# Kernel optimization log

Measured on AMD Instinct MI355X. Metric: run time of the kernel, lower is better.

Reference implementation:

```python
import jax, jax.numpy as jnp
from jax import lax
import numpy as np

GAMMA, ALPHA, BETA, THETA = 0.5, 0.5, 1.0, 1.0
BLOCK = 512  # tile size over the p2 point dim for the streaming K=1 knn


def _min_sqdist(p1, p2):
    """K=1 knn_points: min squared distance from each p1 point to p2. (B,N1,3),(B,N2,3) -> (B,N1).
    Streams p2 in blocks with a running min, never materializing the full NxM matrix."""
    B, N2, _ = p2.shape
    nb = N2 // BLOCK
    p2b = jnp.transpose(p2.reshape(B, nb, BLOCK, 3), (1, 0, 2, 3))  # (nb,B,BLOCK,3)
    p1sq = jnp.sum(p1 * p1, axis=-1)  # (B,N1)

    def step(carry, chunk):
        # ||a-b||^2 = ||a||^2 - 2 a.b + ||b||^2
        d = (p1sq[:, :, None]
             - 2.0 * jnp.einsum('bnd,bmd->bnm', p1, chunk)
             + jnp.sum(chunk * chunk, axis=-1)[:, None, :])
        return jnp.minimum(carry, jnp.min(d, axis=-1)), None

    init = jnp.full(p1sq.shape, jnp.inf, dtype=p1.dtype)
    out, _ = lax.scan(step, init, p2b)
    return out


def _pnt2quat(grasp_pred):
    center = grasp_pred[..., :3]
    q = grasp_pred[..., 3:]
    q = q / jnp.sqrt(jnp.sum(q * q, axis=-1, keepdims=True) + 1e-12)
    return center, q


def _mat2quat(g):
    R = g[..., :3, :3]
    t = g[..., :3, 3]
    tr = R[..., 0, 0] + R[..., 1, 1] + R[..., 2, 2]
    w = 0.5 * jnp.sqrt(jnp.maximum(1.0 + tr, 1e-12))
    inv4w = 1.0 / (4.0 * w)
    x = (R[..., 2, 1] - R[..., 1, 2]) * inv4w
    y = (R[..., 0, 2] - R[..., 2, 0]) * inv4w
    z = (R[..., 1, 0] - R[..., 0, 1]) * inv4w
    q = jnp.stack([w, x, y, z], axis=-1)
    return t, q


def setup_inputs() -> dict:
    key = jax.random.key(0)
    ks = jax.random.split(key, 8)
    B, N, M = 4, 16384, 2048
    xyz = jax.random.normal(ks[0], (B, N, 3), dtype=jnp.float32)
    sample_xyz = jax.random.normal(ks[1], (B, M, 3), dtype=jnp.float32)
    temp = jnp.asarray(0.5, dtype=jnp.float32)
    grasp_pred = jax.random.normal(ks[2], (B, M, 7), dtype=jnp.float32)
    # build valid SE(3) ground-truth grasps: rotation from unit quaternion (w>=0) + translation
    q = jax.random.normal(ks[3], (B, M, 4), dtype=jnp.float32)
    q = q / jnp.sqrt(jnp.sum(q * q, axis=-1, keepdims=True) + 1e-12)
    q = jnp.where(q[..., :1] < 0, -q, q)
    w, x, y, z = q[..., 0], q[..., 1], q[..., 2], q[..., 3]
    R = jnp.stack([
        jnp.stack([1 - 2 * (y * y + z * z), 2 * (x * y - w * z), 2 * (x * z + w * y)], -1),
        jnp.stack([2 * (x * y + w * z), 1 - 2 * (x * x + z * z), 2 * (y * z - w * x)], -1),
        jnp.stack([2 * (x * z - w * y), 2 * (y * z + w * x), 1 - 2 * (x * x + y * y)], -1),
    ], -2)  # (B,M,3,3)
    t = jax.random.normal(ks[4], (B, M, 3), dtype=jnp.float32)
    top = jnp.concatenate([R, t[..., None]], axis=-1)  # (B,M,3,4)
    bottom = jnp.broadcast_to(jnp.array([0., 0., 0., 1.], jnp.float32), (B, M, 1, 4))
    grasp_gt = jnp.concatenate([top, bottom], axis=-2)  # (B,M,4,4)
    class_pred = jax.random.uniform(ks[5], (B, M), dtype=jnp.float32, minval=1e-4, maxval=1.0 - 1e-4)
    class_gt = (jax.random.uniform(ks[6], (B, M)) < 0.5).astype(jnp.float32)
    return {"xyz": xyz, "sample_xyz": sample_xyz, "temp": temp, "grasp_pred": grasp_pred,
            "grasp_gt": grasp_gt, "class_pred": class_pred, "class_gt": class_gt}


def reference(xyz, sample_xyz, temp, grasp_pred, grasp_gt, class_pred, class_gt):
    # sample loss (chamfer-style with K=1 knn in both directions + max-min coverage term)
    d_smp_org = _min_sqdist(sample_xyz, xyz)   # (B,M)
    d_org_smp = _min_sqdist(xyz, sample_xyz)   # (B,N)
    sample_loss = (jnp.mean(d_smp_org)
                   + jnp.mean(jnp.max(d_smp_org, axis=-1))
                   + GAMMA * jnp.mean(d_org_smp))
    # projection loss
    proj_loss = temp ** 2
    center_pred, quat_pred = _pnt2quat(grasp_pred)
    center_gt, quat_gt = _mat2quat(grasp_gt)
    cls_w = class_gt.reshape(-1)
    dist = jnp.linalg.norm(center_pred.reshape(-1, 3) - center_gt.reshape(-1, 3) + 1e-6, axis=-1)
    trans_loss = jnp.mean(dist * cls_w)
    dot = jnp.sum(quat_pred.reshape(-1, 4) * quat_gt.reshape(-1, 4), axis=-1)
    rot = jnp.arccos(jnp.clip(jnp.abs(dot), 0.0, 1.0 - 1e-7))
    rot_loss = jnp.mean(rot * cls_w)
    reg_loss = trans_loss + ALPHA * rot_loss
    # classification loss (BCE on probabilities)
    p = jnp.clip(class_pred, 1e-7, 1.0 - 1e-7)
    cls_loss = -jnp.mean(class_gt * jnp.log(p) + (1.0 - class_gt) * jnp.log(1.0 - p))
    return THETA * sample_loss + proj_loss + BETA * reg_loss + cls_loss
```

## Files before the change

### kernel.cpp

```cpp
#include <hip/hip_runtime.h>
#include <math.h>

#define BB 4
#define NN 16384
#define MM 2048
#define BM (BB*MM)
#define BN (BB*NN)

#define TGT 256
#define S1  64
#define S2  8

#define PART1OFF 0
#define PART2OFF (S1*BM)
#define REDOFF   (PART1OFF + S1*BM + S2*BN)
#define R_SUMS1  (REDOFF)
#define R_MAXES  (REDOFF+32)
#define R_SUMS2  (REDOFF+64)
#define R_GST    (REDOFF+128)
#define R_GSR    (REDOFF+160)
#define R_GSC    (REDOFF+192)

__global__ __launch_bounds__(256) void k_min(const float* __restrict__ xyz,
                                             const float* __restrict__ smp,
                                             float* __restrict__ ws) {
    __shared__ float4 tgt[TGT];
    const int tid = threadIdx.x;
    const int bx  = blockIdx.x;
    const float* qptr; const float* tptr; float* outp;
    if (bx < 256) {
        int b = bx >> 6, r = bx & 63, qb = r >> 3, s = r & 7;
        int gq = b * NN + qb * 2048;
        qptr = xyz + (size_t)gq * 3;
        tptr = smp + (size_t)(b * MM + s * TGT) * 3;
        outp = ws + PART2OFF + s * BN + gq;
    } else {
        int bx2 = bx - 256;
        int b = bx2 >> 6, s = bx2 & 63;
        int gq = b * MM;
        qptr = smp + (size_t)gq * 3;
        tptr = xyz + (size_t)(b * NN + s * TGT) * 3;
        outp = ws + PART1OFF + s * BM + gq;
    }
    {
        float x = tptr[3*tid], y = tptr[3*tid+1], z = tptr[3*tid+2];
        tgt[tid] = make_float4(-2.0f*x, -2.0f*y, -2.0f*z, x*x + y*y + z*z);
    }
    float qx[8], qy[8], qz[8], mn[8];
#pragma unroll
    for (int k = 0; k < 8; ++k) {
        int q = tid + k * 256;
        qx[k] = qptr[3*q]; qy[k] = qptr[3*q+1]; qz[k] = qptr[3*q+2];
        mn[k] = INFINITY;
    }
    __syncthreads();
#pragma unroll 2
    for (int j = 0; j < TGT; j += 2) {
        float4 ta = tgt[j], tb = tgt[j+1];
#pragma unroll
        for (int k = 0; k < 8; ++k) {
            float da = fmaf(ta.x, qx[k], fmaf(ta.y, qy[k], fmaf(ta.z, qz[k], ta.w)));
            float db = fmaf(tb.x, qx[k], fmaf(tb.y, qy[k], fmaf(tb.z, qz[k], tb.w)));
            mn[k] = fminf(mn[k], fminf(da, db));
        }
    }
#pragma unroll
    for (int k = 0; k < 8; ++k) {
        int q = tid + k * 256;
        outp[q] = mn[k] + (qx[k]*qx[k] + qy[k]*qy[k] + qz[k]*qz[k]);
    }
}

__device__ __forceinline__ float blockSum256(float v, volatile float* s4) {
#pragma unroll
    for (int o = 32; o > 0; o >>= 1) v += __shfl_down(v, o, 64);
    __syncthreads();
    int lane = threadIdx.x & 63, w = threadIdx.x >> 6;
    if (lane == 0) s4[w] = v;
    __syncthreads();
    return s4[0] + s4[1] + s4[2] + s4[3];
}

__device__ __forceinline__ float blockMax256(float v, volatile float* s4) {
#pragma unroll
    for (int o = 32; o > 0; o >>= 1) v = fmaxf(v, __shfl_down(v, o, 64));
    __syncthreads();
    int lane = threadIdx.x & 63, w = threadIdx.x >> 6;
    if (lane == 0) s4[w] = v;
    __syncthreads();
    return fmaxf(fmaxf(s4[0], s4[1]), fmaxf(s4[2], s4[3]));
}

__global__ __launch_bounds__(256) void k_reduce(const float* __restrict__ gp,
                                                const float* __restrict__ gg,
                                                const float* __restrict__ cp,
                                                const float* __restrict__ cg,
                                                float* __restrict__ ws) {
    __shared__ float s4a[4], s4b[4], s4c[4];
    const int bx = blockIdx.x, tid = threadIdx.x;
    if (bx < 32) {
        int q = bx * 256 + tid;
        float v = INFINITY;
#pragma unroll
        for (int sp = 0; sp < S1; ++sp) v = fminf(v, ws[PART1OFF + sp * BM + q]);
        float bs = blockSum256(v, s4a);
        float bm = blockMax256(v, s4b);
        if (tid == 0) { ws[R_SUMS1 + bx] = bs; ws[R_MAXES + bx] = bm; }
    } else if (bx < 96) {
        int i = bx - 32;
        float s = 0.0f;
#pragma unroll
        for (int k = 0; k < 4; ++k) {
            int q = i * 1024 + tid + k * 256;
            float v = INFINITY;
#pragma unroll
            for (int sp = 0; sp < S2; ++sp) v = fminf(v, ws[PART2OFF + sp * BN + q]);
            s += v;
        }
        float bs = blockSum256(s, s4a);
        if (tid == 0) ws[R_SUMS2 + i] = bs;
    } else {
        int m = (bx - 96) * 256 + tid;
        const float* g = gp + (size_t)m * 7;
        float cxp = g[0], cyp = g[1], czp = g[2];
        float q0 = g[3], q1 = g[4], q2 = g[5], q3 = g[6];
        float invq = 1.0f / sqrtf(q0*q0 + q1*q1 + q2*q2 + q3*q3 + 1e-12f);
        const float* G = gg + (size_t)m * 16;
        float tr = G[0] + G[5] + G[10];
        float w = 0.5f * sqrtf(fmaxf(1.0f + tr, 1e-12f));
        float inv4w = 1.0f / (4.0f * w);
        float gqx = (G[9] - G[6]) * inv4w;
        float gqy = (G[2] - G[8]) * inv4w;
        float gqz = (G[4] - G[1]) * inv4w;
        float cw = cg[m];
        float dx = cxp - G[3]  + 1e-6f;
        float dy = cyp - G[7]  + 1e-6f;
        float dz = czp - G[11] + 1e-6f;
        float dist = sqrtf(dx*dx + dy*dy + dz*dz);
        float dot = (q0*w + q1*gqx + q2*gqy + q3*gqz) * invq;
        float rot = acosf(fminf(fabsf(dot), 1.0f - 1e-7f));
        float p = fminf(fmaxf(cp[m], 1e-7f), 1.0f - 1e-7f);
        float ce = cw * logf(p) + (1.0f - cw) * logf(1.0f - p);
        float s1 = blockSum256(dist * cw, s4a);
        float s2 = blockSum256(rot  * cw, s4b);
        float s3 = blockSum256(ce, s4c);
        int i = bx - 96;
        if (tid == 0) { ws[R_GST + i] = s1; ws[R_GSR + i] = s2; ws[R_GSC + i] = s3; }
    }
}

__global__ __launch_bounds__(256) void k_final(const float* __restrict__ temp,
                                               const float* __restrict__ ws,
                                               float* __restrict__ out) {
    __shared__ float s4[4];
    const int tid = threadIdx.x;
    float a = (tid < 32) ? ws[R_SUMS1 + tid] : 0.0f;
    float f = 0.0f;
    if (tid < 4) {
        f = -INFINITY;
#pragma unroll
        for (int r = 0; r < 8; ++r) f = fmaxf(f, ws[R_MAXES + tid * 8 + r]);
    }
    float b = (tid < 64) ? ws[R_SUMS2 + tid] : 0.0f;
    float c = (tid < 32) ? ws[R_GST + tid] : 0.0f;
    float d = (tid < 32) ? ws[R_GSR + tid] : 0.0f;
    float e = (tid < 32) ? ws[R_GSC + tid] : 0.0f;
    float A = blockSum256(a, s4);
    float F = blockSum256(f, s4);
    float B = blockSum256(b, s4);
    float C = blockSum256(c, s4);
    float D = blockSum256(d, s4);
    float E = blockSum256(e, s4);
    if (tid == 0) {
        float sample = A * (1.0f / BM) + F * 0.25f + 0.5f * B * (1.0f / BN);
        float reg    = C * (1.0f / BM) + 0.5f * D * (1.0f / BM);
        float cls    = -E * (1.0f / BM);
        float t = temp[0];
        out[0] = sample + t * t + reg + cls;
    }
}

extern "C" void kernel_launch(void* const* d_in, const int* in_sizes, int n_in,
                              void* d_out, int out_size, void* d_ws, size_t ws_size,
                              hipStream_t stream) {
    const float* xyz  = (const float*)d_in[0];
    const float* smp  = (const float*)d_in[1];
    const float* temp = (const float*)d_in[2];
    const float* gp   = (const float*)d_in[3];
    const float* gg   = (const float*)d_in[4];
    const float* cp   = (const float*)d_in[5];
    const float* cg   = (const float*)d_in[6];
    float* ws  = (float*)d_ws;
    float* out = (float*)d_out;

    hipLaunchKernelGGL(k_min,    dim3(512), dim3(256), 0, stream, xyz, smp, ws);
    hipLaunchKernelGGL(k_reduce, dim3(128), dim3(256), 0, stream, gp, gg, cp, cg, ws);
    hipLaunchKernelGGL(k_final,  dim3(1),   dim3(256), 0, stream, temp, ws, out);
}
```

Measured before the change: 97.38 us.

## Use packed FP32 FMAs in knn kernel and fuse final reduction via last-block atomic

The distance inner loop now processes query points in pairs with inline-asm v_pk_fma_f32, using op_sel to broadcast target components, so the FMA instruction count is halved. The separate single-block final kernel is removed. Instead, the last k_reduce block to finish, found with an atomic counter and threadfences, does the final sum. This saves one kernel launch and its tail. The counter is reset inside k_min, and the packed asm relies on correct op_sel semantics.

```diff
diff --git a/kernel.cpp b/kernel.cpp
--- a/kernel.cpp
+++ b/kernel.cpp
@@ -20,6 +20,28 @@
 #define R_GST    (REDOFF+128)
 #define R_GSR    (REDOFF+160)
 #define R_GSC    (REDOFF+192)
+#define R_CNT    (REDOFF+224)
+
+typedef float f2 __attribute__((ext_vector_type(2)));
+
+__device__ __forceinline__ f2 pk_fma_zw(f2 tzw, f2 q) {
+    f2 d;
+    asm("v_pk_fma_f32 %0, %1, %2, %1 op_sel:[0,0,1] op_sel_hi:[0,1,1]"
+        : "=v"(d) : "v"(tzw), "v"(q));
+    return d;
+}
+__device__ __forceinline__ f2 pk_fma_hi(f2 txy, f2 q, f2 c) {
+    f2 d;
+    asm("v_pk_fma_f32 %0, %1, %2, %3 op_sel:[1,0,0] op_sel_hi:[1,1,1]"
+        : "=v"(d) : "v"(txy), "v"(q), "v"(c));
+    return d;
+}
+__device__ __forceinline__ f2 pk_fma_lo(f2 txy, f2 q, f2 c) {
+    f2 d;
+    asm("v_pk_fma_f32 %0, %1, %2, %3 op_sel:[0,0,0] op_sel_hi:[0,1,1]"
+        : "=v"(d) : "v"(txy), "v"(q), "v"(c));
+    return d;
+}
 
 __global__ __launch_bounds__(256) void k_min(const float* __restrict__ xyz,
                                              const float* __restrict__ smp,
@@ -27,6 +49,7 @@
     __shared__ float4 tgt[TGT];
     const int tid = threadIdx.x;
     const int bx  = blockIdx.x;
+    if (bx == 0 && tid == 0) ((unsigned*)ws)[R_CNT] = 0u;
     const float* qptr; const float* tptr; float* outp;
     if (bx < 256) {
         int b = bx >> 6, r = bx & 63, qb = r >> 3, s = r & 7;
@@ -46,28 +69,40 @@
         float x = tptr[3*tid], y = tptr[3*tid+1], z = tptr[3*tid+2];
         tgt[tid] = make_float4(-2.0f*x, -2.0f*y, -2.0f*z, x*x + y*y + z*z);
     }
-    float qx[8], qy[8], qz[8], mn[8];
-#pragma unroll
-    for (int k = 0; k < 8; ++k) {
-        int q = tid + k * 256;
-        qx[k] = qptr[3*q]; qy[k] = qptr[3*q+1]; qz[k] = qptr[3*q+2];
-        mn[k] = INFINITY;
-    }
-    __syncthreads();
+    f2 qx2[4], qy2[4], qz2[4], mn2[4];
+#pragma unroll
+    for (int p = 0; p < 4; ++p) {
+        int qa = tid + (2*p)   * 256;
+        int qb = tid + (2*p+1) * 256;
+        qx2[p] = (f2){qptr[3*qa],   qptr[3*qb]};
+        qy2[p] = (f2){qptr[3*qa+1], qptr[3*qb+1]};
+        qz2[p] = (f2){qptr[3*qa+2], qptr[3*qb+2]};
+        mn2[p] = (f2){INFINITY, INFINITY};
+    }
+    __syncthreads();
+    const f2* tg2 = (const f2*)tgt;
 #pragma unroll 2
     for (int j = 0; j < TGT; j += 2) {
-        float4 ta = tgt[j], tb = tgt[j+1];
-#pragma unroll
-        for (int k = 0; k < 8; ++k) {
-            float da = fmaf(ta.x, qx[k], fmaf(ta.y, qy[k], fmaf(ta.z, qz[k], ta.w)));
-            float db = fmaf(tb.x, qx[k], fmaf(tb.y, qy[k], fmaf(tb.z, qz[k], tb.w)));
-            mn[k] = fminf(mn[k], fminf(da, db));
-        }
-    }
-#pragma unroll
-    for (int k = 0; k < 8; ++k) {
-        int q = tid + k * 256;
-        outp[q] = mn[k] + (qx[k]*qx[k] + qy[k]*qy[k] + qz[k]*qz[k]);
+        f2 taxy = tg2[2*j+0], tazw = tg2[2*j+1];
+        f2 tbxy = tg2[2*j+2], tbzw = tg2[2*j+3];
+#pragma unroll
+        for (int p = 0; p < 4; ++p) {
+            f2 da = pk_fma_zw(tazw, qz2[p]);
+            da = pk_fma_hi(taxy, qy2[p], da);
+            da = pk_fma_lo(taxy, qx2[p], da);
+            f2 db = pk_fma_zw(tbzw, qz2[p]);
+            db = pk_fma_hi(tbxy, qy2[p], db);
+            db = pk_fma_lo(tbxy, qx2[p], db);
+            mn2[p].x = fminf(mn2[p].x, fminf(da.x, db.x));
+            mn2[p].y = fminf(mn2[p].y, fminf(da.y, db.y));
+        }
+    }
+#pragma unroll
+    for (int p = 0; p < 4; ++p) {
+        int qa = tid + (2*p)   * 256;
+        int qb = tid + (2*p+1) * 256;
+        outp[qa] = mn2[p].x + (qx2[p].x*qx2[p].x + qy2[p].x*qy2[p].x + qz2[p].x*qz2[p].x);
+        outp[qb] = mn2[p].y + (qx2[p].y*qx2[p].y + qy2[p].y*qy2[p].y + qz2[p].y*qz2[p].y);
     }
 }
 
@@ -95,8 +130,11 @@
                                                 const float* __restrict__ gg,
                                                 const float* __restrict__ cp,
                                                 const float* __restrict__ cg,
-                                                float* __restrict__ ws) {
+                                                const float* __restrict__ temp,
+                                                float* __restrict__ ws,
+                                                float* __restrict__ out) {
     __shared__ float s4a[4], s4b[4], s4c[4];
+    __shared__ bool amLast;
     const int bx = blockIdx.x, tid = threadIdx.x;
     if (bx < 32) {
         int q = bx * 256 + tid;
@@ -147,36 +185,38 @@
         int i = bx - 96;
         if (tid == 0) { ws[R_GST + i] = s1; ws[R_GSR + i] = s2; ws[R_GSC + i] = s3; }
     }
-}
-
-__global__ __launch_bounds__(256) void k_final(const float* __restrict__ temp,
-                                               const float* __restrict__ ws,
-                                               float* __restrict__ out) {
-    __shared__ float s4[4];
-    const int tid = threadIdx.x;
-    float a = (tid < 32) ? ws[R_SUMS1 + tid] : 0.0f;
-    float f = 0.0f;
-    if (tid < 4) {
-        f = -INFINITY;
-#pragma unroll
-        for (int r = 0; r < 8; ++r) f = fmaxf(f, ws[R_MAXES + tid * 8 + r]);
-    }
-    float b = (tid < 64) ? ws[R_SUMS2 + tid] : 0.0f;
-    float c = (tid < 32) ? ws[R_GST + tid] : 0.0f;
-    float d = (tid < 32) ? ws[R_GSR + tid] : 0.0f;
-    float e = (tid < 32) ? ws[R_GSC + tid] : 0.0f;
-    float A = blockSum256(a, s4);
-    float F = blockSum256(f, s4);
-    float B = blockSum256(b, s4);
-    float C = blockSum256(c, s4);
-    float D = blockSum256(d, s4);
-    float E = blockSum256(e, s4);
+    __threadfence();
     if (tid == 0) {
-        float sample = A * (1.0f / BM) + F * 0.25f + 0.5f * B * (1.0f / BN);
-        float reg    = C * (1.0f / BM) + 0.5f * D * (1.0f / BM);
-        float cls    = -E * (1.0f / BM);
-        float t = temp[0];
-        out[0] = sample + t * t + reg + cls;
+        unsigned prev = atomicAdd((unsigned*)ws + R_CNT, 1u);
+        amLast = (prev == 127u);
+    }
+    __syncthreads();
+    if (amLast) {
+        __threadfence();
+        float a = (tid < 32) ? ws[R_SUMS1 + tid] : 0.0f;
+        float f = 0.0f;
+        if (tid < 4) {
+            f = -INFINITY;
+#pragma unroll
+            for (int r = 0; r < 8; ++r) f = fmaxf(f, ws[R_MAXES + tid * 8 + r]);
+        }
+        float b = (tid < 64) ? ws[R_SUMS2 + tid] : 0.0f;
+        float c = (tid < 32) ? ws[R_GST + tid] : 0.0f;
+        float d = (tid < 32) ? ws[R_GSR + tid] : 0.0f;
+        float e = (tid < 32) ? ws[R_GSC + tid] : 0.0f;
+        float A = blockSum256(a, s4a);
+        float F = blockSum256(f, s4a);
+        float B = blockSum256(b, s4a);
+        float C = blockSum256(c, s4a);
+        float D = blockSum256(d, s4a);
+        float E = blockSum256(e, s4a);
+        if (tid == 0) {
+            float sample = A * (1.0f / BM) + F * 0.25f + 0.5f * B * (1.0f / BN);
+            float reg    = C * (1.0f / BM) + 0.5f * D * (1.0f / BM);
+            float cls    = -E * (1.0f / BM);
+            float t = temp[0];
+            out[0] = sample + t * t + reg + cls;
+        }
     }
 }
 
@@ -194,6 +234,5 @@
     float* out = (float*)d_out;
 
     hipLaunchKernelGGL(k_min,    dim3(512), dim3(256), 0, stream, xyz, smp, ws);
-    hipLaunchKernelGGL(k_reduce, dim3(128), dim3(256), 0, stream, gp, gg, cp, cg, ws);
-    hipLaunchKernelGGL(k_final,  dim3(1),   dim3(256), 0, stream, temp, ws, out);
-}
+    hipLaunchKernelGGL(k_reduce, dim3(128), dim3(256), 0, stream, gp, gg, cp, cg, temp, ws, out);
+}
```

Measured after the change: 109.4 us. +12.3%, slower.

## Fuse grasp loss into min kernel and finalize via last-block atomic counter

Applied to the files above, without the earlier changes.

Moves the per-grasp regression and classification loss blocks into the knn min kernel as 32 extra blocks, and merges the final scalar reduction into the reduce kernel using a threadfence plus atomic counter so the last block finishes. This cuts the launch count from three to two and spreads the partial-min reduction over more blocks (128 instead of 64 for the N side). The counter is reset by block 0 of the first kernel, which relies on stream ordering, and the added fences and atomics add some overhead.

```diff
diff --git a/kernel.cpp b/kernel.cpp
--- a/kernel.cpp
+++ b/kernel.cpp
@@ -17,110 +17,46 @@
 #define R_SUMS1  (REDOFF)
 #define R_MAXES  (REDOFF+32)
 #define R_SUMS2  (REDOFF+64)
-#define R_GST    (REDOFF+128)
-#define R_GSR    (REDOFF+160)
-#define R_GSC    (REDOFF+192)
+#define R_GST    (REDOFF+192)
+#define R_GSR    (REDOFF+224)
+#define R_GSC    (REDOFF+256)
+#define R_CNT    (REDOFF+288)
+
+__device__ __forceinline__ float blockSum256(float v, volatile float* s4) {
+#pragma unroll
+    for (int o = 32; o > 0; o >>= 1) v += __shfl_down(v, o, 64);
+    __syncthreads();
+    int lane = threadIdx.x & 63, w = threadIdx.x >> 6;
+    if (lane == 0) s4[w] = v;
+    __syncthreads();
+    return s4[0] + s4[1] + s4[2] + s4[3];
+}
+
+__device__ __forceinline__ float blockMax256(float v, volatile float* s4) {
+#pragma unroll
+    for (int o = 32; o > 0; o >>= 1) v = fmaxf(v, __shfl_down(v, o, 64));
+    __syncthreads();
+    int lane = threadIdx.x & 63, w = threadIdx.x >> 6;
+    if (lane == 0) s4[w] = v;
+    __syncthreads();
+    return fmaxf(fmaxf(s4[0], s4[1]), fmaxf(s4[2], s4[3]));
+}
 
 __global__ __launch_bounds__(256) void k_min(const float* __restrict__ xyz,
                                              const float* __restrict__ smp,
+                                             const float* __restrict__ gp,
+                                             const float* __restrict__ gg,
+                                             const float* __restrict__ cp,
+                                             const float* __restrict__ cg,
                                              float* __restrict__ ws) {
     __shared__ float4 tgt[TGT];
+    __shared__ float s4a[4], s4b[4], s4c[4];
     const int tid = threadIdx.x;
     const int bx  = blockIdx.x;
-    const float* qptr; const float* tptr; float* outp;
-    if (bx < 256) {
-        int b = bx >> 6, r = bx & 63, qb = r >> 3, s = r & 7;
-        int gq = b * NN + qb * 2048;
-        qptr = xyz + (size_t)gq * 3;
-        tptr = smp + (size_t)(b * MM + s * TGT) * 3;
-        outp = ws + PART2OFF + s * BN + gq;
-    } else {
-        int bx2 = bx - 256;
-        int b = bx2 >> 6, s = bx2 & 63;
-        int gq = b * MM;
-        qptr = smp + (size_t)gq * 3;
-        tptr = xyz + (size_t)(b * NN + s * TGT) * 3;
-        outp = ws + PART1OFF + s * BM + gq;
-    }
-    {
-        float x = tptr[3*tid], y = tptr[3*tid+1], z = tptr[3*tid+2];
-        tgt[tid] = make_float4(-2.0f*x, -2.0f*y, -2.0f*z, x*x + y*y + z*z);
-    }
-    float qx[8], qy[8], qz[8], mn[8];
-#pragma unroll
-    for (int k = 0; k < 8; ++k) {
-        int q = tid + k * 256;
-        qx[k] = qptr[3*q]; qy[k] = qptr[3*q+1]; qz[k] = qptr[3*q+2];
-        mn[k] = INFINITY;
-    }
-    __syncthreads();
-#pragma unroll 2
-    for (int j = 0; j < TGT; j += 2) {
-        float4 ta = tgt[j], tb = tgt[j+1];
-#pragma unroll
-        for (int k = 0; k < 8; ++k) {
-            float da = fmaf(ta.x, qx[k], fmaf(ta.y, qy[k], fmaf(ta.z, qz[k], ta.w)));
-            float db = fmaf(tb.x, qx[k], fmaf(tb.y, qy[k], fmaf(tb.z, qz[k], tb.w)));
-            mn[k] = fminf(mn[k], fminf(da, db));
-        }
-    }
-#pragma unroll
-    for (int k = 0; k < 8; ++k) {
-        int q = tid + k * 256;
-        outp[q] = mn[k] + (qx[k]*qx[k] + qy[k]*qy[k] + qz[k]*qz[k]);
-    }
-}
-
-__device__ __forceinline__ float blockSum256(float v, volatile float* s4) {
-#pragma unroll
-    for (int o = 32; o > 0; o >>= 1) v += __shfl_down(v, o, 64);
-    __syncthreads();
-    int lane = threadIdx.x & 63, w = threadIdx.x >> 6;
-    if (lane == 0) s4[w] = v;
-    __syncthreads();
-    return s4[0] + s4[1] + s4[2] + s4[3];
-}
-
-__device__ __forceinline__ float blockMax256(float v, volatile float* s4) {
-#pragma unroll
-    for (int o = 32; o > 0; o >>= 1) v = fmaxf(v, __shfl_down(v, o, 64));
-    __syncthreads();
-    int lane = threadIdx.x & 63, w = threadIdx.x >> 6;
-    if (lane == 0) s4[w] = v;
-    __syncthreads();
-    return fmaxf(fmaxf(s4[0], s4[1]), fmaxf(s4[2], s4[3]));
-}
-
-__global__ __launch_bounds__(256) void k_reduce(const float* __restrict__ gp,
-                                                const float* __restrict__ gg,
-                                                const float* __restrict__ cp,
-                                                const float* __restrict__ cg,
-                                                float* __restrict__ ws) {
-    __shared__ float s4a[4], s4b[4], s4c[4];
-    const int bx = blockIdx.x, tid = threadIdx.x;
-    if (bx < 32) {
-        int q = bx * 256 + tid;
-        float v = INFINITY;
-#pragma unroll
-        for (int sp = 0; sp < S1; ++sp) v = fminf(v, ws[PART1OFF + sp * BM + q]);
-        float bs = blockSum256(v, s4a);
-        float bm = blockMax256(v, s4b);
-        if (tid == 0) { ws[R_SUMS1 + bx] = bs; ws[R_MAXES + bx] = bm; }
-    } else if (bx < 96) {
-        int i = bx - 32;
-        float s = 0.0f;
-#pragma unroll
-        for (int k = 0; k < 4; ++k) {
-            int q = i * 1024 + tid + k * 256;
-            float v = INFINITY;
-#pragma unroll
-            for (int sp = 0; sp < S2; ++sp) v = fminf(v, ws[PART2OFF + sp * BN + q]);
-            s += v;
-        }
-        float bs = blockSum256(s, s4a);
-        if (tid == 0) ws[R_SUMS2 + i] = bs;
-    } else {
-        int m = (bx - 96) * 256 + tid;
+    if (bx == 0 && tid == 0) ((unsigned*)ws)[R_CNT] = 0u;
+
+    if (bx >= 512) {
+        int m = (bx - 512) * 256 + tid;
         const float* g = gp + (size_t)m * 7;
         float cxp = g[0], cyp = g[1], czp = g[2];
         float q0 = g[3], q1 = g[4], q2 = g[5], q3 = g[6];
@@ -144,39 +80,115 @@
         float s1 = blockSum256(dist * cw, s4a);
         float s2 = blockSum256(rot  * cw, s4b);
         float s3 = blockSum256(ce, s4c);
-        int i = bx - 96;
+        int i = bx - 512;
         if (tid == 0) { ws[R_GST + i] = s1; ws[R_GSR + i] = s2; ws[R_GSC + i] = s3; }
-    }
-}
-
-__global__ __launch_bounds__(256) void k_final(const float* __restrict__ temp,
-                                               const float* __restrict__ ws,
-                                               float* __restrict__ out) {
-    __shared__ float s4[4];
-    const int tid = threadIdx.x;
-    float a = (tid < 32) ? ws[R_SUMS1 + tid] : 0.0f;
-    float f = 0.0f;
-    if (tid < 4) {
-        f = -INFINITY;
-#pragma unroll
-        for (int r = 0; r < 8; ++r) f = fmaxf(f, ws[R_MAXES + tid * 8 + r]);
-    }
-    float b = (tid < 64) ? ws[R_SUMS2 + tid] : 0.0f;
-    float c = (tid < 32) ? ws[R_GST + tid] : 0.0f;
-    float d = (tid < 32) ? ws[R_GSR + tid] : 0.0f;
-    float e = (tid < 32) ? ws[R_GSC + tid] : 0.0f;
-    float A = blockSum256(a, s4);
-    float F = blockSum256(f, s4);
-    float B = blockSum256(b, s4);
-    float C = blockSum256(c, s4);
-    float D = blockSum256(d, s4);
-    float E = blockSum256(e, s4);
+        return;
+    }
+
+    const float* qptr; const float* tptr; float* outp;
+    if (bx < 256) {
+        int b = bx >> 6, r = bx & 63, qb = r >> 3, s = r & 7;
+        int gq = b * NN + qb * 2048;
+        qptr = xyz + (size_t)gq * 3;
+        tptr = smp + (size_t)(b * MM + s * TGT) * 3;
+        outp = ws + PART2OFF + s * BN + gq;
+    } else {
+        int bx2 = bx - 256;
+        int b = bx2 >> 6, s = bx2 & 63;
+        int gq = b * MM;
+        qptr = smp + (size_t)gq * 3;
+        tptr = xyz + (size_t)(b * NN + s * TGT) * 3;
+        outp = ws + PART1OFF + s * BM + gq;
+    }
+    {
+        float x = tptr[3*tid], y = tptr[3*tid+1], z = tptr[3*tid+2];
+        tgt[tid] = make_float4(-2.0f*x, -2.0f*y, -2.0f*z, x*x + y*y + z*z);
+    }
+    float qx[8], qy[8], qz[8], mn[8];
+#pragma unroll
+    for (int k = 0; k < 8; ++k) {
+        int q = tid + k * 256;
+        qx[k] = qptr[3*q]; qy[k] = qptr[3*q+1]; qz[k] = qptr[3*q+2];
+        mn[k] = INFINITY;
+    }
+    __syncthreads();
+#pragma unroll 2
+    for (int j = 0; j < TGT; j += 2) {
+        float4 ta = tgt[j], tb = tgt[j+1];
+#pragma unroll
+        for (int k = 0; k < 8; ++k) {
+            float da = fmaf(ta.x, qx[k], fmaf(ta.y, qy[k], fmaf(ta.z, qz[k], ta.w)));
+            float db = fmaf(tb.x, qx[k], fmaf(tb.y, qy[k], fmaf(tb.z, qz[k], tb.w)));
+            mn[k] = fminf(mn[k], fminf(da, db));
+        }
+    }
+#pragma unroll
+    for (int k = 0; k < 8; ++k) {
+        int q = tid + k * 256;
+        outp[q] = mn[k] + (qx[k]*qx[k] + qy[k]*qy[k] + qz[k]*qz[k]);
+    }
+}
+
+__global__ __launch_bounds__(256) void k_reduce(const float* __restrict__ temp,
+                                                float* __restrict__ ws,
+                                                float* __restrict__ out) {
+    __shared__ float s4a[4], s4b[4];
+    __shared__ bool amLast;
+    const int bx = blockIdx.x, tid = threadIdx.x;
+    if (bx < 32) {
+        int q = bx * 256 + tid;
+        float v = INFINITY;
+#pragma unroll
+        for (int sp = 0; sp < S1; ++sp) v = fminf(v, ws[PART1OFF + sp * BM + q]);
+        float bs = blockSum256(v, s4a);
+        float bm = blockMax256(v, s4b);
+        if (tid == 0) { ws[R_SUMS1 + bx] = bs; ws[R_MAXES + bx] = bm; }
+    } else {
+        int i = bx - 32;
+        float s = 0.0f;
+#pragma unroll
+        for (int k = 0; k < 2; ++k) {
+            int q = i * 512 + tid + k * 256;
+            float v = INFINITY;
+#pragma unroll
+            for (int sp = 0; sp < S2; ++sp) v = fminf(v, ws[PART2OFF + sp * BN + q]);
+            s += v;
+        }
+        float bs = blockSum256(s, s4a);
+        if (tid == 0) ws[R_SUMS2 + i] = bs;
+    }
+    __threadfence();
     if (tid == 0) {
-        float sample = A * (1.0f / BM) + F * 0.25f + 0.5f * B * (1.0f / BN);
-        float reg    = C * (1.0f / BM) + 0.5f * D * (1.0f / BM);
-        float cls    = -E * (1.0f / BM);
-        float t = temp[0];
-        out[0] = sample + t * t + reg + cls;
+        unsigned prev = atomicAdd((unsigned*)ws + R_CNT, 1u);
+        amLast = (prev == 159u);
+    }
+    __syncthreads();
+    if (amLast) {
+        __threadfence();
+        float a = (tid < 32) ? ws[R_SUMS1 + tid] : 0.0f;
+        float f = 0.0f;
+        if (tid < 4) {
+            f = -INFINITY;
+#pragma unroll
+            for (int r = 0; r < 8; ++r) f = fmaxf(f, ws[R_MAXES + tid * 8 + r]);
+        }
+        float b = (tid < 128) ? ws[R_SUMS2 + tid] : 0.0f;
+        float c = (tid < 32) ? ws[R_GST + tid] : 0.0f;
+        float d = (tid < 32) ? ws[R_GSR + tid] : 0.0f;
+        float e = (tid < 32) ? ws[R_GSC + tid] : 0.0f;
+        float A = blockSum256(a, s4a);
+        float F = blockSum256(f, s4a);
+        float B = blockSum256(b, s4a);
+        float C = blockSum256(c, s4a);
+        float D = blockSum256(d, s4a);
+        float E = blockSum256(e, s4a);
+        if (tid == 0) {
+            float sample = A * (1.0f / BM) + F * 0.25f + 0.5f * B * (1.0f / BN);
+            float reg    = C * (1.0f / BM) + 0.5f * D * (1.0f / BM);
+            float cls    = -E * (1.0f / BM);
+            float t = temp[0];
+            out[0] = sample + t * t + reg + cls;
+        }
     }
 }
 
@@ -193,7 +205,7 @@
     float* ws  = (float*)d_ws;
     float* out = (float*)d_out;
 
-    hipLaunchKernelGGL(k_min,    dim3(512), dim3(256), 0, stream, xyz, smp, ws);
-    hipLaunchKernelGGL(k_reduce, dim3(128), dim3(256), 0, stream, gp, gg, cp, cg, ws);
-    hipLaunchKernelGGL(k_final,  dim3(1),   dim3(256), 0, stream, temp, ws, out);
-}
+    hipLaunchKernelGGL(k_min,    dim3(544), dim3(256), 0, stream,
+                       xyz, smp, gp, gg, cp, cg, ws);
+    hipLaunchKernelGGL(k_reduce, dim3(160), dim3(256), 0, stream, temp, ws, out);
+}
```

Measured after the change: 109.5 us. 12.4% more time.
